# Performance work log

Measured on AMD Instinct MI355X. Metric: run time of the kernel, lower is better.

The kernel has to match this reference:

```python
import jax, jax.numpy as jnp
import numpy as np

B, T, V, H, C = 128, 4096, 128, 256, 10
EPS = 0.1  # args._epsilon (training mode)

def setup_inputs() -> dict:
    key = jax.random.key(0)
    ks = jax.random.split(key, 8)
    rn = lambda k, shape, sc: (jax.random.normal(k, shape, jnp.float32) * sc)
    return {
        "X": rn(ks[0], (B, T, V), 1.0),
        "u": jax.random.uniform(ks[1], (B, T, 1), jnp.float32),
        "Wk": rn(ks[2], (V, 4 * H), 0.05),
        "Wr": rn(ks[3], (H, 4 * H), 0.05),
        "b_lstm": jnp.zeros((4 * H,), jnp.float32),
        "Wo": rn(ks[4], (H, C), 0.05),
        "bo": jnp.zeros((C,), jnp.float32),
        "Wc": rn(ks[5], (H + 1, 1), 0.05),
        "bc": jnp.zeros((1,), jnp.float32),
        "Wb": rn(ks[6], (H + 1, 1), 0.05),
        "bb": jnp.zeros((1,), jnp.float32),
    }

def reference(X, u, Wk, Wr, b_lstm, Wo, bo, Wc, bc, Wb, bb):
    Bn = X.shape[0]
    xT = jnp.swapaxes(X, 0, 1)  # [T,B,V]
    uT = jnp.swapaxes(u, 0, 1)  # [T,B,1]
    ts = jnp.arange(T, dtype=jnp.float32)

    def step(carry, inp):
        h, c, preds, halt = carry
        x_t, u_t, t = inp
        # Keras LSTMCell: gates order i, f, g(c), o
        z = x_t @ Wk + h @ Wr + b_lstm  # [B,4H]
        i, f, g, o = jnp.split(z, 4, axis=1)
        i = jax.nn.sigmoid(i); f = jax.nn.sigmoid(f)
        g = jnp.tanh(g); o = jax.nn.sigmoid(o)
        c = f * c + i * g
        h = o * jnp.tanh(c)
        logits = jax.nn.softmax(h @ Wo + bo, axis=-1)  # softmax Dense
        time = jnp.ones((Bn, 1), jnp.float32) * t
        c_in = jax.lax.stop_gradient(jnp.concatenate([h, time], axis=1))
        p = jax.nn.sigmoid(c_in @ Wc + bc)
        probs = (1.0 - EPS) * p + EPS * 0.05
        a = (u_t < probs).astype(jnp.float32)  # Bernoulli sample via uniform noise
        _b = c_in @ Wb + bb  # baseline (does not affect returned logits)
        preds = jnp.where((a == 1.0) & (preds == 0.0), logits, preds)
        halt = jnp.where((halt == -1.0) & (a == 1.0), time, halt)
        return (h, c, preds, halt), logits

    init = (jnp.zeros((Bn, H), jnp.float32),
            jnp.zeros((Bn, H), jnp.float32),
            jnp.zeros((Bn, C), jnp.float32),
            -jnp.ones((Bn, 1), jnp.float32))
    (h, c, preds, halt), all_logits = jax.lax.scan(step, init, (xT, uT, ts))
    logits_last = all_logits[-1]
    # samples that never halted get the final-step logits
    return jnp.where(preds == 0.0, logits_last, preds)
```

## Files before the change

### kernel.cpp

```cpp
#include <hip/hip_runtime.h>
#include <cstddef>
#include <cstdint>

#define NT_ 4096
#define NV_ 128
#define NH_ 256
#define NC_ 10
#define KT_ 384
#define NGRP 16
#define SB   8
#define GWG  16
#define TPW  256
#define VST  12
#define Z9   9
#define FULLMASK 255

#define SM_W    0
#define SM_V    24576
#define SM_ZP   (SM_V + KT_*VST)
#define SM_C    (SM_ZP + 2304)
#define SM_BL   (SM_C + 144)
#define SM_WC   (SM_BL + 64)
#define SM_WO   (SM_WC + 260)
#define SM_HD   (SM_WO + 2560)
#define SM_RED  (SM_HD + 12)
#define SM_TOT  (SM_RED + 32)
#define SMEM_BYTES (SM_TOT * 4)

#define WS_HBUF  65536
#define WS_DIAG  (1u << 20)

#define ALD(p)    __hip_atomic_load((p), __ATOMIC_RELAXED, __HIP_MEMORY_SCOPE_AGENT)
#define AST(p,v)  __hip_atomic_store((p), (v), __ATOMIC_RELAXED, __HIP_MEMORY_SCOPE_AGENT)

#define FMA8(S) \
  acc[S].x = fmaf(w4.x, vs, acc[S].x); \
  acc[S].y = fmaf(w4.y, vs, acc[S].y); \
  acc[S].z = fmaf(w4.z, vs, acc[S].z); \
  acc[S].w = fmaf(w4.w, vs, acc[S].w);

#define ZSTEP(i)                                            \
  {                                                         \
    float4 w4 = wl4[(i) * 256 + wbase];                     \
    const float* vk = v_lds + ((i) * 16 + ks) * VST;        \
    float4 va = *(const float4*)(vk);                       \
    float4 vb = *(const float4*)(vk + 4);                   \
    { float vs = va.x; FMA8(0) } { float vs = va.y; FMA8(1) } \
    { float vs = va.z; FMA8(2) } { float vs = va.w; FMA8(3) } \
    { float vs = vb.x; FMA8(4) } { float vs = vb.y; FMA8(5) } \
    { float vs = vb.z; FMA8(6) } { float vs = vb.w; FMA8(7) } \
  }

extern "C" __global__ __launch_bounds__(TPW, 1)
void earliest_coop(const float* __restrict__ X, const float* __restrict__ U,
                   const float* __restrict__ Wk, const float* __restrict__ Wr,
                   const float* __restrict__ bl, const float* __restrict__ Wo,
                   const float* __restrict__ bo, const float* __restrict__ Wc,
                   const float* __restrict__ bc, float* __restrict__ out,
                   int* __restrict__ tags, float* __restrict__ hbuf,
                   char* __restrict__ diag)
{
  extern __shared__ float smem[];
  float* w_lds = smem + SM_W;
  float* v_lds = smem + SM_V;
  float* zp    = smem + SM_ZP;
  float* c_lds = smem + SM_C;
  float* bl_s  = smem + SM_BL;
  float* wc_s  = smem + SM_WC;
  float* wo_s  = smem + SM_WO;
  float* hd_s  = smem + SM_HD;
  float* red   = smem + SM_RED;
  __shared__ int halted_lds;
  __shared__ int wflags;

  const int tid  = threadIdx.x;
  const int w    = blockIdx.x & 15;
  const int g    = blockIdx.x >> 4;
  const int colq = tid & 15;
  const int ks   = tid >> 4;
  const bool leader = (w == 0);

  for (int m = 0; m < 24; ++m) {
    int idx4 = m * 256 + tid;
    int k = idx4 >> 4, cq = idx4 & 15;
    int rr = cq >> 2, qq = cq & 3;
    int col4 = rr * 64 + w * 4 + qq;
    float4 wv;
    if (k < NV_) wv = ((const float4*)Wk)[(size_t)k * 256 + col4];
    else         wv = ((const float4*)Wr)[(size_t)(k - NV_) * 256 + col4];
    ((float4*)w_lds)[k * 16 + (cq ^ (k & 7))] = wv;
  }
  if (tid < 64) {
    int rr = tid >> 4, e = tid & 15;
    bl_s[tid] = bl[rr * 256 + w * 16 + e];
  }
  wc_s[tid] = Wc[tid];
  if (tid == 0) wc_s[256] = Wc[256];
  if (tid < 128) c_lds[(tid >> 3) * Z9 + (tid & 7)] = 0.f;
  if (leader) {
    for (int m = tid; m < NH_ * NC_; m += TPW) wo_s[m] = Wo[m];
  }
  if (tid < 10)  hd_s[tid] = bo[tid];
  if (tid == 10) hd_s[10] = bc[0];
  if (tid == 0)  { halted_lds = 0; wflags = 0; }

  int* tag_me   = tags + (g << 10) + (w << 6);
  int* tag_poll = tags + (g << 10) + ((tid & 15) << 6);
  const int cswz  = colq ^ (ks & 7);
  const int wbase = ks * 16 + cswz;
  const float4* wl4 = (const float4*)w_lds;

  const int xk4 = tid >> 3;
  const int xs  = tid & 7;
  const float4* X4 = (const float4*)X;
  float4 xr = X4[((size_t)(g * SB + xs) * NT_ + 0) * 32 + xk4];

  const int he0 = tid >> 1;
  const int hs0 = (tid & 1) * 4;

  __syncthreads();
  {
    #pragma unroll
    for (int j = 0; j < 4; ++j)
      v_lds[(4 * xk4 + j) * VST + xs] = ((const float*)&xr)[j];
  }
  __syncthreads();

  float4 acc[8];
  #pragma unroll
  for (int s = 0; s < 8; ++s) acc[s] = make_float4(0.f, 0.f, 0.f, 0.f);
  #pragma unroll
  for (int i = 0; i < 8; ++i) ZSTEP(i)

  float uv_pf = 0.f;

  for (int it = 0;; ++it) {
    if (tid == 0) wflags = 0;
    if (it == 0) {
      #pragma unroll
      for (int i2 = 0; i2 < 8; ++i2) {
        int flat = i2 * 256 + tid;
        v_lds[(NV_ + (flat >> 3)) * VST + (flat & 7)] = 0.f;
      }
    } else {
      const float4* hsrc4 = (const float4*)(hbuf + ((size_t)(it & 1) * NGRP + g) * NH_ * SB);
      const float4* p0 = hsrc4 + tid;
      const float4* p1 = p0 + 256;
      float4 a0, a1;
      asm volatile(
        "global_load_dwordx4 %0, %2, off sc1\n\t"
        "global_load_dwordx4 %1, %3, off sc1\n\t"
        "s_waitcnt vmcnt(0)"
        : "=&v"(a0), "=&v"(a1) : "v"(p0), "v"(p1) : "memory");
      *(float4*)(v_lds + (NV_ + he0) * VST + hs0)       = a0;
      *(float4*)(v_lds + (NV_ + 128 + he0) * VST + hs0) = a1;
    }
    __syncthreads();

    if (it < NT_) {
      if (it + 1 < NT_)
        xr = X4[((size_t)(g * SB + xs) * NT_ + (it + 1)) * 32 + xk4];
      #pragma unroll
      for (int i = 8; i < 24; ++i) ZSTEP(i)
      #pragma unroll
      for (int off = 16; off <= 32; off <<= 1) {
        #pragma unroll
        for (int s = 0; s < 8; ++s) {
          acc[s].x += __shfl_xor(acc[s].x, off, 64);
          acc[s].y += __shfl_xor(acc[s].y, off, 64);
          acc[s].z += __shfl_xor(acc[s].z, off, 64);
          acc[s].w += __shfl_xor(acc[s].w, off, 64);
        }
      }
      if ((tid & 48) == 0) {
        int w4 = tid >> 6;
        float4* zp4 = (float4*)zp;
        #pragma unroll
        for (int s = 0; s < 8; ++s) zp4[(w4 * 16 + colq) * Z9 + s] = acc[s];
      }
    }
    if (it >= 1) {
      const float* hv = v_lds + (NV_ + tid) * VST;
      const float wcv = wc_s[tid];
      float part[SB];
      #pragma unroll
      for (int s = 0; s < SB; ++s) part[s] = hv[s] * wcv;
      #pragma unroll
      for (int off = 1; off <= 32; off <<= 1) {
        #pragma unroll
        for (int s = 0; s < SB; ++s) part[s] += __shfl_xor(part[s], off, 64);
      }
      if ((tid & 63) == 0) {
        int w4 = tid >> 6;
        #pragma unroll
        for (int s = 0; s < SB; ++s) red[w4 * 8 + s] = part[s];
      }
      if (tid >= 128 && tid < 128 + SB)
        uv_pf = U[(size_t)(g * SB + (tid - 128)) * NT_ + (it - 1)];
    }
    __syncthreads();

    if (it < NT_ && tid < 128) {
      int e = tid >> 3, s = tid & 7;
      float zg4[4];
      #pragma unroll
      for (int r = 0; r < 4; ++r) {
        int cq = r * 4 + (e >> 2);
        int j  = e & 3;
        float sum = 0.f;
        #pragma unroll
        for (int w4 = 0; w4 < 4; ++w4)
          sum += zp[((w4 * 16 + cq) * Z9 + s) * 4 + j];
        zg4[r] = sum + bl_s[r * 16 + e];
      }
      float gi = 1.f / (1.f + expf(-zg4[0]));
      float gf = 1.f / (1.f + expf(-zg4[1]));
      float gg = tanhf(zg4[2]);
      float go = 1.f / (1.f + expf(-zg4[3]));
      float c = gf * c_lds[e * Z9 + s] + gi * gg;
      c_lds[e * Z9 + s] = c;
      float h = go * tanhf(c);
      size_t hidx = (((size_t)((it + 1) & 1) * NGRP + g) * NH_ + (w * 16 + e)) * SB + s;
      AST(hbuf + hidx, h);
    }
    if (it >= 1 && tid >= 128 && tid < 128 + SB) {
      const int s_ = tid - 128;
      if (!((halted_lds >> s_) & 1)) {
        const int tau = it - 1;
        const float psum = red[0 * 8 + s_] + red[1 * 8 + s_] + red[2 * 8 + s_] + red[3 * 8 + s_];
        const float pre   = psum + (float)tau * wc_s[256] + hd_s[10];
        const float p     = 1.f / (1.f + expf(-pre));
        const float probs = 0.9f * p + 0.005f;
        const bool  a     = (uv_pf < probs);
        if (a || tau == NT_ - 1) atomicOr(&wflags, 1 << s_);
        if (a) atomicOr(&halted_lds, 1 << s_);
      }
    }
    __syncthreads();

    if (tid == 0) {
      AST(tag_me, it + 1);
      if (diag)
        __builtin_nontemporal_store(1u,
            (uint32_t*)(diag + (((size_t)blockIdx.x << 8) + (it & 255)) * 64));
    }

    if (it + 1 < NT_) {
      #pragma unroll
      for (int j = 0; j < 4; ++j)
        v_lds[(4 * xk4 + j) * VST + xs] = ((const float*)&xr)[j];
    }

    if (it >= 1 && leader && wflags) {
      const int e5 = tid >> 3, s = tid & 7;
      float accv[NC_];
      #pragma unroll
      for (int cc = 0; cc < NC_; ++cc) accv[cc] = 0.f;
      #pragma unroll
      for (int i2 = 0; i2 < 8; ++i2) {
        const int e = i2 * 32 + e5;
        const float hvv = v_lds[(NV_ + e) * VST + s];
        #pragma unroll
        for (int cc = 0; cc < NC_; ++cc) accv[cc] += hvv * wo_s[e * NC_ + cc];
      }
      #pragma unroll
      for (int off = 8; off <= 32; off <<= 1) {
        #pragma unroll
        for (int cc = 0; cc < NC_; ++cc) accv[cc] += __shfl_xor(accv[cc], off, 64);
      }
      if ((tid & 56) == 0) {
        const int w4 = tid >> 6;
        #pragma unroll
        for (int cc = 0; cc < NC_; ++cc) zp[(w4 * 8 + s) * NC_ + cc] = accv[cc];
      }
      __syncthreads();
      if (tid < SB && ((wflags >> tid) & 1)) {
        const int s_ = tid;
        float l[NC_];
        float mx = -1e30f;
        #pragma unroll
        for (int cc = 0; cc < NC_; ++cc) {
          l[cc] = zp[(0 * 8 + s_) * NC_ + cc] + zp[(1 * 8 + s_) * NC_ + cc]
                + zp[(2 * 8 + s_) * NC_ + cc] + zp[(3 * 8 + s_) * NC_ + cc] + hd_s[cc];
          mx = fmaxf(mx, l[cc]);
        }
        float ssum = 0.f;
        #pragma unroll
        for (int cc = 0; cc < NC_; ++cc) { l[cc] = expf(l[cc] - mx); ssum += l[cc]; }
        const float inv = 1.f / ssum;
        float* op = out + (g * SB + s_) * NC_;
        #pragma unroll
        for (int cc = 0; cc < NC_; ++cc) op[cc] = l[cc] * inv;
      }
      __syncthreads();
    }

    if (halted_lds == FULLMASK || it == NT_) break;

    __syncthreads();

    #pragma unroll
    for (int s = 0; s < 8; ++s) acc[s] = make_float4(0.f, 0.f, 0.f, 0.f);
    if (it + 1 < NT_) {
      #pragma unroll
      for (int i = 0; i < 8; ++i) ZSTEP(i)
    }

    if (tid < 64) {
      const int target = it + 1;
      for (;;) {
        int tv = ALD(tag_poll);
        if (__all(tv >= target)) break;
        __builtin_amdgcn_s_sleep(1);
      }
    }
    __syncthreads();
  }
}

extern "C" void kernel_launch(void* const* d_in, const int* in_sizes, int n_in,
                              void* d_out, int out_size, void* d_ws, size_t ws_size,
                              hipStream_t stream)
{
  const float* X  = (const float*)d_in[0];
  const float* U  = (const float*)d_in[1];
  const float* Wk = (const float*)d_in[2];
  const float* Wr = (const float*)d_in[3];
  const float* bL = (const float*)d_in[4];
  const float* Wo = (const float*)d_in[5];
  const float* bo = (const float*)d_in[6];
  const float* Wc = (const float*)d_in[7];
  const float* bc = (const float*)d_in[8];
  float* out = (float*)d_out;

  int*   tags = (int*)d_ws;
  float* hbuf = (float*)((char*)d_ws + WS_HBUF);
  char*  diag = (ws_size >= (6u << 20)) ? ((char*)d_ws + WS_DIAG) : nullptr;

  hipMemsetAsync(d_ws, 0, WS_HBUF, stream);

  hipFuncSetAttribute((const void*)earliest_coop,
                      hipFuncAttributeMaxDynamicSharedMemorySize, SMEM_BYTES);

  void* args[] = { (void*)&X, (void*)&U, (void*)&Wk, (void*)&Wr, (void*)&bL,
                   (void*)&Wo, (void*)&bo, (void*)&Wc, (void*)&bc, (void*)&out,
                   (void*)&tags, (void*)&hbuf, (void*)&diag };
  hipError_t lerr = hipLaunchCooperativeKernel((const void*)earliest_coop,
                                               dim3(NGRP * GWG), dim3(TPW),
                                               args, SMEM_BYTES, stream);
  if (lerr != hipSuccess) {
    hipLaunchKernelGGL(earliest_coop, dim3(NGRP * GWG), dim3(TPW), SMEM_BYTES, stream,
                       X, U, Wk, Wr, bL, Wo, bo, Wc, bc, out, tags, hbuf, diag);
  }
}
```

Baseline: 172.6 us.

## Overlap h-state global load with input-projection partial and drop a barrier

Moves the load of the previous step's hidden state from the top of the loop to right after the cross-workgroup tag wait. The load is issued asynchronously and the x-part ZSTEP FMAs run while it is in flight, with the waitcnt placed only before the LDS store. One __syncthreads per iteration is removed, and the zero-initialisation of the h slice moves before the loop. It also adds memrealtime-based timing of the wait and writes it into a diag2 buffer when the workspace is large enough, which costs some extra instructions.

```diff
diff --git a/kernel.cpp b/kernel.cpp
--- a/kernel.cpp
+++ b/kernel.cpp
@@ -29,6 +29,7 @@
 
 #define WS_HBUF  65536
 #define WS_DIAG  (1u << 20)
+#define WS_DIAG2 (16u << 20)
 
 #define ALD(p)    __hip_atomic_load((p), __ATOMIC_RELAXED, __HIP_MEMORY_SCOPE_AGENT)
 #define AST(p,v)  __hip_atomic_store((p), (v), __ATOMIC_RELAXED, __HIP_MEMORY_SCOPE_AGENT)
@@ -58,7 +59,7 @@
                    const float* __restrict__ bo, const float* __restrict__ Wc,
                    const float* __restrict__ bc, float* __restrict__ out,
                    int* __restrict__ tags, float* __restrict__ hbuf,
-                   char* __restrict__ diag)
+                   char* __restrict__ diag, char* __restrict__ diag2)
 {
   extern __shared__ float smem[];
   float* w_lds = smem + SM_W;
@@ -124,6 +125,13 @@
     for (int j = 0; j < 4; ++j)
       v_lds[(4 * xk4 + j) * VST + xs] = ((const float*)&xr)[j];
   }
+  {
+    #pragma unroll
+    for (int i2 = 0; i2 < 8; ++i2) {
+      int flat = i2 * 256 + tid;
+      v_lds[(NV_ + (flat >> 3)) * VST + (flat & 7)] = 0.f;
+    }
+  }
   __syncthreads();
 
   float4 acc[8];
@@ -133,29 +141,13 @@
   for (int i = 0; i < 8; ++i) ZSTEP(i)
 
   float uv_pf = 0.f;
+  unsigned long long t0 = 0, cum = 0;
 
   for (int it = 0;; ++it) {
-    if (tid == 0) wflags = 0;
-    if (it == 0) {
-      #pragma unroll
-      for (int i2 = 0; i2 < 8; ++i2) {
-        int flat = i2 * 256 + tid;
-        v_lds[(NV_ + (flat >> 3)) * VST + (flat & 7)] = 0.f;
-      }
-    } else {
-      const float4* hsrc4 = (const float4*)(hbuf + ((size_t)(it & 1) * NGRP + g) * NH_ * SB);
-      const float4* p0 = hsrc4 + tid;
-      const float4* p1 = p0 + 256;
-      float4 a0, a1;
-      asm volatile(
-        "global_load_dwordx4 %0, %2, off sc1\n\t"
-        "global_load_dwordx4 %1, %3, off sc1\n\t"
-        "s_waitcnt vmcnt(0)"
-        : "=&v"(a0), "=&v"(a1) : "v"(p0), "v"(p1) : "memory");
-      *(float4*)(v_lds + (NV_ + he0) * VST + hs0)       = a0;
-      *(float4*)(v_lds + (NV_ + 128 + he0) * VST + hs0) = a1;
-    }
     __syncthreads();
+    if (tid == 0 && it >= 1)
+      cum += __builtin_amdgcn_s_memrealtime() - t0;
+    if (tid == 192) wflags = 0;
 
     if (it < NT_) {
       if (it + 1 < NT_)
@@ -239,18 +231,17 @@
     __syncthreads();
 
     if (tid == 0) {
+      t0 = __builtin_amdgcn_s_memrealtime();
       AST(tag_me, it + 1);
       if (diag)
         __builtin_nontemporal_store(1u,
             (uint32_t*)(diag + (((size_t)blockIdx.x << 8) + (it & 255)) * 64));
     }
-
     if (it + 1 < NT_) {
       #pragma unroll
       for (int j = 0; j < 4; ++j)
         v_lds[(4 * xk4 + j) * VST + xs] = ((const float*)&xr)[j];
     }
-
     if (it >= 1 && leader && wflags) {
       const int e5 = tid >> 3, s = tid & 7;
       float accv[NC_];
@@ -297,15 +288,6 @@
 
     if (halted_lds == FULLMASK || it == NT_) break;
 
-    __syncthreads();
-
-    #pragma unroll
-    for (int s = 0; s < 8; ++s) acc[s] = make_float4(0.f, 0.f, 0.f, 0.f);
-    if (it + 1 < NT_) {
-      #pragma unroll
-      for (int i = 0; i < 8; ++i) ZSTEP(i)
-    }
-
     if (tid < 64) {
       const int target = it + 1;
       for (;;) {
@@ -315,6 +297,34 @@
       }
     }
     __syncthreads();
+
+    {
+      const float4* hsrc4 = (const float4*)(hbuf + ((size_t)((it + 1) & 1) * NGRP + g) * NH_ * SB);
+      const float4* p0 = hsrc4 + tid;
+      const float4* p1 = p0 + 256;
+      float4 a0, a1;
+      asm volatile(
+        "global_load_dwordx4 %0, %2, off sc1\n\t"
+        "global_load_dwordx4 %1, %3, off sc1"
+        : "=&v"(a0), "=&v"(a1) : "v"(p0), "v"(p1) : "memory");
+      #pragma unroll
+      for (int s = 0; s < 8; ++s) acc[s] = make_float4(0.f, 0.f, 0.f, 0.f);
+      if (it + 1 < NT_) {
+        #pragma unroll
+        for (int i = 0; i < 8; ++i) ZSTEP(i)
+      }
+      asm volatile("s_waitcnt vmcnt(0)" ::: "memory");
+      *(float4*)(v_lds + (NV_ + he0) * VST + hs0)       = a0;
+      *(float4*)(v_lds + (NV_ + 128 + he0) * VST + hs0) = a1;
+    }
+  }
+
+  if (tid == 0 && diag2) {
+    long long n = (long long)(cum >> 8);
+    if (n > 1023) n = 1023;
+    for (long long i = 0; i < n; ++i)
+      __builtin_nontemporal_store(1u,
+          (uint32_t*)(diag2 + ((size_t)blockIdx.x << 16) + (size_t)i * 64));
   }
 }
 
@@ -333,9 +343,10 @@
   const float* bc = (const float*)d_in[8];
   float* out = (float*)d_out;
 
-  int*   tags = (int*)d_ws;
-  float* hbuf = (float*)((char*)d_ws + WS_HBUF);
-  char*  diag = (ws_size >= (6u << 20)) ? ((char*)d_ws + WS_DIAG) : nullptr;
+  int*   tags  = (int*)d_ws;
+  float* hbuf  = (float*)((char*)d_ws + WS_HBUF);
+  char*  diag  = (ws_size >= (6u  << 20)) ? ((char*)d_ws + WS_DIAG)  : nullptr;
+  char*  diag2 = (ws_size >= (64u << 20)) ? ((char*)d_ws + WS_DIAG2) : nullptr;
 
   hipMemsetAsync(d_ws, 0, WS_HBUF, stream);
 
@@ -344,12 +355,12 @@
 
   void* args[] = { (void*)&X, (void*)&U, (void*)&Wk, (void*)&Wr, (void*)&bL,
                    (void*)&Wo, (void*)&bo, (void*)&Wc, (void*)&bc, (void*)&out,
-                   (void*)&tags, (void*)&hbuf, (void*)&diag };
+                   (void*)&tags, (void*)&hbuf, (void*)&diag, (void*)&diag2 };
   hipError_t lerr = hipLaunchCooperativeKernel((const void*)earliest_coop,
                                                dim3(NGRP * GWG), dim3(TPW),
                                                args, SMEM_BYTES, stream);
   if (lerr != hipSuccess) {
     hipLaunchKernelGGL(earliest_coop, dim3(NGRP * GWG), dim3(TPW), SMEM_BYTES, stream,
-                       X, U, Wk, Wr, bL, Wo, bo, Wc, bc, out, tags, hbuf, diag);
+                       X, U, Wk, Wr, bL, Wo, bo, Wc, bc, out, tags, hbuf, diag, diag2);
   }
 }
```

After: 170.9 us. Within noise of the previous version (-1.0%).

## Fetch each peer's hidden-state slice as soon as its tag arrives

Applied to the files above, without the earlier changes.

The per-step hidden-state exchange now overlaps with the barrier wait. The polling wavefront checks which peer workgroups have published their tags and immediately issues loads for those workgroups' slices, instead of waiting for all tags and then loading the whole h vector at the top of the next iteration. The h region in LDS moves to a dense 8-wide layout so the loaded float2 pieces can be stored directly, and one barrier per step is removed. It also changes the diagnostic store pattern and moves the precomputed x-part ZSTEP after the wait. The risks are extra register use for 16 pending loads and possible visibility ordering issues between the relaxed tag load and the data load.

```diff
diff --git a/kernel.cpp b/kernel.cpp
--- a/kernel.cpp
+++ b/kernel.cpp
@@ -6,18 +6,18 @@
 #define NV_ 128
 #define NH_ 256
 #define NC_ 10
-#define KT_ 384
 #define NGRP 16
 #define SB   8
 #define GWG  16
 #define TPW  256
 #define VST  12
+#define VH   1536
 #define Z9   9
 #define FULLMASK 255
 
 #define SM_W    0
 #define SM_V    24576
-#define SM_ZP   (SM_V + KT_*VST)
+#define SM_ZP   (SM_V + 4608)
 #define SM_C    (SM_ZP + 2304)
 #define SM_BL   (SM_C + 144)
 #define SM_WC   (SM_BL + 64)
@@ -39,16 +39,17 @@
   acc[S].z = fmaf(w4.z, vs, acc[S].z); \
   acc[S].w = fmaf(w4.w, vs, acc[S].w);
 
-#define ZSTEP(i)                                            \
-  {                                                         \
-    float4 w4 = wl4[(i) * 256 + wbase];                     \
-    const float* vk = v_lds + ((i) * 16 + ks) * VST;        \
-    float4 va = *(const float4*)(vk);                       \
-    float4 vb = *(const float4*)(vk + 4);                   \
-    { float vs = va.x; FMA8(0) } { float vs = va.y; FMA8(1) } \
-    { float vs = va.z; FMA8(2) } { float vs = va.w; FMA8(3) } \
-    { float vs = vb.x; FMA8(4) } { float vs = vb.y; FMA8(5) } \
-    { float vs = vb.z; FMA8(6) } { float vs = vb.w; FMA8(7) } \
+#define ZSTEP(i)                                                          \
+  {                                                                       \
+    float4 w4 = wl4[(i) * 256 + wbase];                                   \
+    const float* vk = ((i) < 8) ? (v_lds + ((i) * 16 + ks) * VST)         \
+                                : (v_lds + VH + (((i) - 8) * 16 + ks) * 8); \
+    float4 va = *(const float4*)(vk);                                     \
+    float4 vb = *(const float4*)(vk + 4);                                 \
+    { float vs = va.x; FMA8(0) } { float vs = va.y; FMA8(1) }             \
+    { float vs = va.z; FMA8(2) } { float vs = va.w; FMA8(3) }             \
+    { float vs = vb.x; FMA8(4) } { float vs = vb.y; FMA8(5) }             \
+    { float vs = vb.z; FMA8(6) } { float vs = vb.w; FMA8(7) }             \
   }
 
 extern "C" __global__ __launch_bounds__(TPW, 1)
@@ -106,23 +107,22 @@
 
   int* tag_me   = tags + (g << 10) + (w << 6);
   int* tag_poll = tags + (g << 10) + ((tid & 15) << 6);
-  const int cswz  = colq ^ (ks & 7);
-  const int wbase = ks * 16 + cswz;
+  const int wbase = ks * 16 + (colq ^ (ks & 7));
   const float4* wl4 = (const float4*)w_lds;
 
   const int xk4 = tid >> 3;
   const int xs  = tid & 7;
   const float4* X4 = (const float4*)X;
   float4 xr = X4[((size_t)(g * SB + xs) * NT_ + 0) * 32 + xk4];
-
-  const int he0 = tid >> 1;
-  const int hs0 = (tid & 1) * 4;
 
   __syncthreads();
   {
     #pragma unroll
     for (int j = 0; j < 4; ++j)
       v_lds[(4 * xk4 + j) * VST + xs] = ((const float*)&xr)[j];
+    #pragma unroll
+    for (int j = 0; j < 8; ++j)
+      v_lds[VH + tid * 8 + j] = 0.f;
   }
   __syncthreads();
 
@@ -135,27 +135,7 @@
   float uv_pf = 0.f;
 
   for (int it = 0;; ++it) {
-    if (tid == 0) wflags = 0;
-    if (it == 0) {
-      #pragma unroll
-      for (int i2 = 0; i2 < 8; ++i2) {
-        int flat = i2 * 256 + tid;
-        v_lds[(NV_ + (flat >> 3)) * VST + (flat & 7)] = 0.f;
-      }
-    } else {
-      const float4* hsrc4 = (const float4*)(hbuf + ((size_t)(it & 1) * NGRP + g) * NH_ * SB);
-      const float4* p0 = hsrc4 + tid;
-      const float4* p1 = p0 + 256;
-      float4 a0, a1;
-      asm volatile(
-        "global_load_dwordx4 %0, %2, off sc1\n\t"
-        "global_load_dwordx4 %1, %3, off sc1\n\t"
-        "s_waitcnt vmcnt(0)"
-        : "=&v"(a0), "=&v"(a1) : "v"(p0), "v"(p1) : "memory");
-      *(float4*)(v_lds + (NV_ + he0) * VST + hs0)       = a0;
-      *(float4*)(v_lds + (NV_ + 128 + he0) * VST + hs0) = a1;
-    }
-    __syncthreads();
+    if (tid == 192) wflags = 0;
 
     if (it < NT_) {
       if (it + 1 < NT_)
@@ -180,7 +160,7 @@
       }
     }
     if (it >= 1) {
-      const float* hv = v_lds + (NV_ + tid) * VST;
+      const float* hv = v_lds + VH + tid * 8;
       const float wcv = wc_s[tid];
       float part[SB];
       #pragma unroll
@@ -240,17 +220,17 @@
 
     if (tid == 0) {
       AST(tag_me, it + 1);
-      if (diag)
-        __builtin_nontemporal_store(1u,
-            (uint32_t*)(diag + (((size_t)blockIdx.x << 8) + (it & 255)) * 64));
-    }
-
+      if (diag && it >= 8 && it < 128) {
+        char* dl = diag + (((size_t)blockIdx.x) << 14) + (size_t)(it - 8) * 128;
+        __builtin_nontemporal_store(1u, (uint32_t*)dl);
+        __builtin_nontemporal_store(1u, (uint32_t*)(dl + 64));
+      }
+    }
     if (it + 1 < NT_) {
       #pragma unroll
       for (int j = 0; j < 4; ++j)
         v_lds[(4 * xk4 + j) * VST + xs] = ((const float*)&xr)[j];
     }
-
     if (it >= 1 && leader && wflags) {
       const int e5 = tid >> 3, s = tid & 7;
       float accv[NC_];
@@ -259,7 +239,7 @@
       #pragma unroll
       for (int i2 = 0; i2 < 8; ++i2) {
         const int e = i2 * 32 + e5;
-        const float hvv = v_lds[(NV_ + e) * VST + s];
+        const float hvv = v_lds[VH + e * 8 + s];
         #pragma unroll
         for (int cc = 0; cc < NC_; ++cc) accv[cc] += hvv * wo_s[e * NC_ + cc];
       }
@@ -297,6 +277,35 @@
 
     if (halted_lds == FULLMASK || it == NT_) break;
 
+    if (tid < 64) {
+      const int target = it + 1;
+      const float2* hsrc2 =
+          (const float2*)(hbuf + ((size_t)((it + 1) & 1) * NGRP + g) * NH_ * SB);
+      float2 sr[16];
+      unsigned pending = 0xffffu;
+      for (;;) {
+        int tv = ALD(tag_poll);
+        unsigned fresh = (unsigned)(__ballot(tv >= target) & 0xffffull);
+        unsigned newly = fresh & pending;
+        if (newly) {
+          #pragma unroll
+          for (int p = 0; p < 16; ++p) {
+            if ((newly >> p) & 1) {
+              const float2* ap = hsrc2 + p * 64 + tid;
+              asm volatile("global_load_dwordx2 %0, %1, off sc1"
+                           : "=&v"(sr[p]) : "v"(ap) : "memory");
+            }
+          }
+          pending &= ~newly;
+        }
+        if (!pending) break;
+        __builtin_amdgcn_s_sleep(1);
+      }
+      asm volatile("s_waitcnt vmcnt(0)" ::: "memory");
+      #pragma unroll
+      for (int p = 0; p < 16; ++p)
+        *(float2*)(v_lds + VH + p * 128 + tid * 2) = sr[p];
+    }
     __syncthreads();
 
     #pragma unroll
@@ -305,16 +314,6 @@
       #pragma unroll
       for (int i = 0; i < 8; ++i) ZSTEP(i)
     }
-
-    if (tid < 64) {
-      const int target = it + 1;
-      for (;;) {
-        int tv = ALD(tag_poll);
-        if (__all(tv >= target)) break;
-        __builtin_amdgcn_s_sleep(1);
-      }
-    }
-    __syncthreads();
   }
 }
 
```

Result: slower. 177.7 us (+3.0%).
